# Optimization experiments

Hardware: AMD Instinct MI355X
Metric: run time of the kernel (lower is better)

The kernel has to match this reference:

```python
import jax, jax.numpy as jnp
import numpy as np

KSIZE = 15
SIGMA = 3.0
PAD = KSIZE // 2


def _gauss_kernel2d():
    g = jnp.arange(KSIZE, dtype=jnp.float32) - KSIZE // 2
    g = jnp.exp(-(g ** 2) / (2.0 * SIGMA * SIGMA))
    g = g / g.sum()
    return g[:, None] * g[None, :]  # [15,15]


def _depthwise_blur(x, k2):
    # x: [B,C,H,W]; 15x15 Gaussian applied per channel (matches per-channel F.conv2d loop)
    C = x.shape[1]
    kernel = jnp.broadcast_to(k2[None, None], (C, 1, KSIZE, KSIZE))
    return jax.lax.conv_general_dilated(
        x, kernel, window_strides=(1, 1), padding=[(PAD, PAD), (PAD, PAD)],
        feature_group_count=C, dimension_numbers=("NCHW", "OIHW", "NCHW"))


def setup_inputs() -> dict:
    key = jax.random.key(0)
    B, C, H, W = 4, 3, 1024, 1024
    x = jax.random.uniform(key, (B, C, H, W), dtype=jnp.float32)
    f32 = lambda v: jnp.asarray(v, dtype=jnp.float32)
    return {
        "x": x,
        "gains": jnp.array([1.1, 1.0, 0.9], dtype=jnp.float32),
        "gamma": f32(0.9),
        "shadow_boost": f32(0.1),
        "highlight_reduce": f32(0.1),
        "brightness": f32(0.05),
        "contrast": f32(1.1),
        "enhance_amount": f32(0.8),
        "softness": f32(0.6),
        "intensity": f32(0.3),
        "rotation": f32(30.0),
        "hardness": f32(2.0),
    }


def reference(x, gains, gamma, shadow_boost, highlight_reduce, brightness,
              contrast, enhance_amount, softness, intensity, rotation, hardness):
    B, C, H, W = x.shape
    k2 = _gauss_kernel2d()

    # WhiteBalanceAdjustment
    x = x * gains.reshape(1, C, 1, 1)
    # ToneCurveAdjustment
    x = jnp.power(x, gamma)
    # ShadowHighlightEnhancement
    hi = jax.nn.sigmoid((x - 0.5) * 10.0)
    x = jnp.clip(x + shadow_boost * (1.0 - hi) - highlight_reduce * hi, 0.0, 1.0)
    # GlobalBrightnessContrastAdjustment
    x = jnp.clip(contrast * (x - 0.5) + 0.5 + brightness, 0.0, 1.0)
    # LocalContrastEnhancement
    local_mean = _depthwise_blur(x, k2)
    x = x + enhance_amount * (x - local_mean)
    # SoftnessFilter
    blurred = _depthwise_blur(x, k2)
    x = softness * blurred + (1.0 - softness) * x
    # GradientNDAdjustment
    ys = jnp.linspace(-1.0, 1.0, H, dtype=jnp.float32)
    xs = jnp.linspace(-1.0, 1.0, W, dtype=jnp.float32)
    grid_y, grid_x = jnp.meshgrid(ys, xs, indexing="ij")
    theta = rotation * (np.pi / 180.0)
    grid_rot = grid_x * jnp.cos(theta) + grid_y * jnp.sin(theta)
    mask = jax.nn.sigmoid(-hardness * grid_rot)[None, None]  # [1,1,H,W]
    x = jnp.clip(x * (1.0 - intensity * mask), 0.0, 1.0)

    return jnp.clip(x, 0.0, 1.0)
```

## Files before the change

### kernel.cpp

```cpp
#include <hip/hip_runtime.h>
#include <math.h>

#define HH 1024
#define WW 1024
#define NPLANES 12
#define PLANE (HH * WW)
#define NTOT (NPLANES * PLANE)

#define TW 64
#define TH 64
#define HRA 78
#define RAWP 84
#define HBLP 68

#define TH2 128
#define HRB 142

struct W15 { float w[15]; };

__device__ inline float4 ld4z(const float* __restrict__ row, int x) {
    if (x >= 0 && x + 3 < WW) return *(const float4*)(row + x);
    float4 r; float* p = (float*)&r;
#pragma unroll
    for (int j = 0; j < 4; ++j) { int xx = x + j; p[j] = (xx >= 0 && xx < WW) ? row[xx] : 0.0f; }
    return r;
}

__device__ inline float chain1(float t, float gain, float gamma, float sb,
                               float hr, float br, float ct) {
    t = t * gain;
    t = __builtin_amdgcn_exp2f(gamma * __log2f(t));
    float hi = __fdividef(1.0f, 1.0f + __expf((0.5f - t) * 10.0f));
    t = t + sb * (1.0f - hi) - hr * hi;
    t = fminf(fmaxf(t, 0.0f), 1.0f);
    t = ct * (t - 0.5f) + 0.5f + br;
    return fminf(fmaxf(t, 0.0f), 1.0f);
}

__global__ __launch_bounds__(256) void k_chain_blur_lce(
    const float* __restrict__ x, float* __restrict__ dst,
    const float* __restrict__ gains,
    const float* __restrict__ pg, const float* __restrict__ psb,
    const float* __restrict__ phr, const float* __restrict__ pbr,
    const float* __restrict__ pct, const float* __restrict__ penh, W15 wk)
{
    __shared__ float raw[HRA * RAWP];
    __shared__ float hbl[HRA * HBLP];
    const int p   = blockIdx.z;
    const int x0  = blockIdx.x * TW;
    const int y0  = blockIdx.y * TH;
    const int tid = threadIdx.x;
    const float* plane = x + (size_t)p * PLANE;

    const float gain  = gains[p % 3];
    const float gamma = *pg, sb = *psb, hr = *phr, br = *pbr, ct = *pct;
    const float e     = *penh;

    for (int i = tid; i < HRA * 20; i += 256) {
        int r  = i / 20;
        int c4 = i % 20;
        int y  = y0 - 7 + r;
        int xb = x0 - 8 + c4 * 4;
        float4 v;
        if (y >= 0 && y < HH) {
            float4 f = ld4z(plane + (size_t)y * WW, xb);
            float* pf = (float*)&f; float* pv = (float*)&v;
#pragma unroll
            for (int j = 0; j < 4; ++j) {
                float cv = chain1(pf[j], gain, gamma, sb, hr, br, ct);
                int xx = xb + j;
                pv[j] = (xx >= 0 && xx < WW) ? cv : 0.0f;
            }
        } else {
            v = make_float4(0.0f, 0.0f, 0.0f, 0.0f);
        }
        *(float4*)&raw[r * RAWP + c4 * 4] = v;
    }
    __syncthreads();

    {
        const int c4 = (tid & 15) * 4;
        const int r0 = tid >> 4;
#pragma unroll
        for (int it = 0; it < 5; ++it) {
            int r = r0 + 16 * it;
            if (r < HRA) {
                float f[20];
#pragma unroll
                for (int m = 0; m < 5; ++m)
                    *(float4*)&f[4 * m] = *(const float4*)&raw[r * RAWP + c4 + 4 * m];
                float4 o; float* po = (float*)&o;
#pragma unroll
                for (int j = 0; j < 4; ++j) {
                    float acc = 0.0f;
#pragma unroll
                    for (int k = 0; k < 15; ++k) acc += wk.w[k] * f[j + 1 + k];
                    po[j] = acc;
                }
                *(float4*)&hbl[r * HBLP + c4] = o;
            }
        }
    }
    __syncthreads();

    const int tx  = tid & 63;
    const int ty  = tid >> 6;
    const int ly0 = ty * 16;

    float win[15];
#pragma unroll
    for (int k = 0; k < 15; ++k) win[k] = hbl[(ly0 + k) * HBLP + tx];

    float* dstP = dst + (size_t)p * PLANE;
#pragma unroll
    for (int j = 0; j < 16; ++j) {
        int y = y0 + ly0 + j;
        float lm = 0.0f;
#pragma unroll
        for (int k = 0; k < 15; ++k) lm += wk.w[k] * win[k];
        float c = raw[(ly0 + j + 7) * RAWP + tx + 8];
        dstP[(size_t)y * WW + x0 + tx] = (1.0f + e) * c - e * lm;
#pragma unroll
        for (int k = 0; k < 14; ++k) win[k] = win[k + 1];
        win[14] = hbl[(ly0 + j + 15) * HBLP + tx];
    }
}

__global__ __launch_bounds__(256) void k_blur_final(
    const float* __restrict__ src, float* __restrict__ dst,
    const float* __restrict__ psoft, const float* __restrict__ pint,
    const float* __restrict__ prot, const float* __restrict__ phard, W15 wk)
{
    __shared__ float hbl[HRB * HBLP];
    const int p   = blockIdx.z;
    const int x0  = blockIdx.x * TW;
    const int y0  = blockIdx.y * TH2;
    const int tid = threadIdx.x;
    const float* plane = src + (size_t)p * PLANE;

    {
        const int c4 = (tid & 15) * 4;
        const int r0 = tid >> 4;
#pragma unroll
        for (int it = 0; it < 9; ++it) {
            int r = r0 + 16 * it;
            if (r < HRB) {
                int y = y0 - 7 + r;
                float4 o;
                if (y >= 0 && y < HH) {
                    const float* row = plane + (size_t)y * WW;
                    int xb = x0 + c4 - 8;
                    float f[20];
                    *(float4*)&f[0]  = ld4z(row, xb);
                    *(float4*)&f[4]  = ld4z(row, xb + 4);
                    *(float4*)&f[8]  = ld4z(row, xb + 8);
                    *(float4*)&f[12] = ld4z(row, xb + 12);
                    *(float4*)&f[16] = ld4z(row, xb + 16);
                    float* po = (float*)&o;
#pragma unroll
                    for (int j = 0; j < 4; ++j) {
                        float acc = 0.0f;
#pragma unroll
                        for (int k = 0; k < 15; ++k) acc += wk.w[k] * f[j + 1 + k];
                        po[j] = acc;
                    }
                } else {
                    o = make_float4(0.0f, 0.0f, 0.0f, 0.0f);
                }
                *(float4*)&hbl[r * HBLP + c4] = o;
            }
        }
    }
    __syncthreads();

    const int tx  = tid & 63;
    const int ty  = tid >> 6;
    const int ly0 = ty * 32;
    const int x   = x0 + tx;

    const float s     = *psoft;
    const float inten = *pint;
    const float hard  = *phard;
    const float theta = (*prot) * 0.017453292519943295f;
    const float cth = __cosf(theta), sth = __sinf(theta);
    const float base = (-1.0f + 2.0f * (float)x * (1.0f / (float)(WW - 1))) * cth;

    float win[15];
#pragma unroll
    for (int k = 0; k < 15; ++k) win[k] = hbl[(ly0 + k) * HBLP + tx];

    float* dstP = dst + (size_t)p * PLANE;
#pragma unroll
    for (int j = 0; j < 32; ++j) {
        int y = y0 + ly0 + j;
        float bl = 0.0f;
#pragma unroll
        for (int k = 0; k < 15; ++k) bl += wk.w[k] * win[k];
        float c = plane[(size_t)y * WW + x];
        float v = s * bl + (1.0f - s) * c;
        float gy = -1.0f + 2.0f * (float)y * (1.0f / (float)(HH - 1));
        float mask = __fdividef(1.0f, 1.0f + __expf(hard * (base + gy * sth)));
        v = v * (1.0f - inten * mask);
        v = fminf(fmaxf(v, 0.0f), 1.0f);
        dstP[(size_t)y * WW + x] = v;
#pragma unroll
        for (int k = 0; k < 14; ++k) win[k] = win[k + 1];
        win[14] = hbl[(ly0 + j + 15) * HBLP + tx];
    }
}

extern "C" void kernel_launch(void* const* d_in, const int* in_sizes, int n_in,
                              void* d_out, int out_size, void* d_ws, size_t ws_size,
                              hipStream_t stream)
{
    const float* x       = (const float*)d_in[0];
    const float* gains   = (const float*)d_in[1];
    const float* p_gamma = (const float*)d_in[2];
    const float* p_sb    = (const float*)d_in[3];
    const float* p_hr    = (const float*)d_in[4];
    const float* p_br    = (const float*)d_in[5];
    const float* p_ct    = (const float*)d_in[6];
    const float* p_enh   = (const float*)d_in[7];
    const float* p_soft  = (const float*)d_in[8];
    const float* p_int   = (const float*)d_in[9];
    const float* p_rot   = (const float*)d_in[10];
    const float* p_hard  = (const float*)d_in[11];

    float* X2  = (float*)d_ws;
    float* OUT = (float*)d_out;

    W15 wk;
    {
        double g[15], sum = 0.0;
        for (int i = 0; i < 15; ++i) { double d = (double)(i - 7); g[i] = exp(-d * d / 18.0); sum += g[i]; }
        for (int i = 0; i < 15; ++i) wk.w[i] = (float)(g[i] / sum);
    }

    dim3 ga(WW / TW, HH / TH, NPLANES);
    k_chain_blur_lce<<<ga, dim3(256), 0, stream>>>(
        x, X2, gains, p_gamma, p_sb, p_hr, p_br, p_ct, p_enh, wk);

    dim3 gb(WW / TW, HH / TH2, NPLANES);
    k_blur_final<<<gb, dim3(256), 0, stream>>>(
        X2, OUT, p_soft, p_int, p_rot, p_hard, wk);
}
```

Baseline: 203.0 us.

## Fuse both blur stages into one kernel with halo recomputation in LDS

Merges the two kernels into a single kernel that computes the tone chain, the first blur and the local-contrast result for a tile with a 14-pixel halo, keeps that intermediate in shared memory, then applies the second blur and the final mask. This removes the global round trip of the intermediate image and one kernel launch. In exchange each 64x32 tile recomputes a large halo (60x96 raw region for 32 output rows), adding redundant chain and blur arithmetic, and uses more shared memory per block, which may limit occupancy.

```diff
diff --git a/kernel.cpp b/kernel.cpp
--- a/kernel.cpp
+++ b/kernel.cpp
@@ -5,16 +5,18 @@
 #define WW 1024
 #define NPLANES 12
 #define PLANE (HH * WW)
-#define NTOT (NPLANES * PLANE)
 
 #define TW 64
-#define TH 64
-#define HRA 78
-#define RAWP 84
-#define HBLP 68
-
-#define TH2 128
-#define HRB 142
+#define TH 32
+#define RAWR 60
+#define RAWC 24
+#define RAWP 100
+#define HB1R 60
+#define HB1P 80
+#define X2R  46
+#define X2P  80
+#define HB2R 46
+#define HB2P 68
 
 struct W15 { float w[15]; };
 
@@ -37,15 +39,20 @@
     return fminf(fmaxf(t, 0.0f), 1.0f);
 }
 
-__global__ __launch_bounds__(256) void k_chain_blur_lce(
-    const float* __restrict__ x, float* __restrict__ dst,
+__global__ __launch_bounds__(256, 2) void k_mega(
+    const float* __restrict__ x, float* __restrict__ out,
     const float* __restrict__ gains,
     const float* __restrict__ pg, const float* __restrict__ psb,
     const float* __restrict__ phr, const float* __restrict__ pbr,
-    const float* __restrict__ pct, const float* __restrict__ penh, W15 wk)
+    const float* __restrict__ pct, const float* __restrict__ penh,
+    const float* __restrict__ psoft, const float* __restrict__ pint,
+    const float* __restrict__ prot, const float* __restrict__ phard, W15 wk)
 {
-    __shared__ float raw[HRA * RAWP];
-    __shared__ float hbl[HRA * HBLP];
+    __shared__ float raw[RAWR * RAWP];
+    __shared__ float hb1[HB1R * HB1P];
+    __shared__ float x2 [X2R  * X2P ];
+    float* hb2 = raw;
+
     const int p   = blockIdx.z;
     const int x0  = blockIdx.x * TW;
     const int y0  = blockIdx.y * TH;
@@ -56,14 +63,14 @@
     const float gamma = *pg, sb = *psb, hr = *phr, br = *pbr, ct = *pct;
     const float e     = *penh;
 
-    for (int i = tid; i < HRA * 20; i += 256) {
-        int r  = i / 20;
-        int c4 = i % 20;
-        int y  = y0 - 7 + r;
-        int xb = x0 - 8 + c4 * 4;
+    for (int i = tid; i < RAWR * RAWC; i += 256) {
+        int r  = i / RAWC;
+        int cc = i - r * RAWC;
+        int gy = y0 - 14 + r;
+        int xb = x0 - 16 + cc * 4;
         float4 v;
-        if (y >= 0 && y < HH) {
-            float4 f = ld4z(plane + (size_t)y * WW, xb);
+        if (gy >= 0 && gy < HH) {
+            float4 f = ld4z(plane + (size_t)gy * WW, xb);
             float* pf = (float*)&f; float* pv = (float*)&v;
 #pragma unroll
             for (int j = 0; j < 4; ++j) {
@@ -74,7 +81,7 @@
         } else {
             v = make_float4(0.0f, 0.0f, 0.0f, 0.0f);
         }
-        *(float4*)&raw[r * RAWP + c4 * 4] = v;
+        *(float4*)&raw[r * RAWP + cc * 4] = v;
     }
     __syncthreads();
 
@@ -82,9 +89,9 @@
         const int c4 = (tid & 15) * 4;
         const int r0 = tid >> 4;
 #pragma unroll
-        for (int it = 0; it < 5; ++it) {
+        for (int it = 0; it < 4; ++it) {
             int r = r0 + 16 * it;
-            if (r < HRA) {
+            if (r < HB1R) {
                 float f[20];
 #pragma unroll
                 for (int m = 0; m < 5; ++m)
@@ -97,115 +104,119 @@
                     for (int k = 0; k < 15; ++k) acc += wk.w[k] * f[j + 1 + k];
                     po[j] = acc;
                 }
-                *(float4*)&hbl[r * HBLP + c4] = o;
-            }
-        }
-    }
-    __syncthreads();
-
-    const int tx  = tid & 63;
-    const int ty  = tid >> 6;
-    const int ly0 = ty * 16;
-
-    float win[15];
-#pragma unroll
-    for (int k = 0; k < 15; ++k) win[k] = hbl[(ly0 + k) * HBLP + tx];
-
-    float* dstP = dst + (size_t)p * PLANE;
-#pragma unroll
-    for (int j = 0; j < 16; ++j) {
-        int y = y0 + ly0 + j;
-        float lm = 0.0f;
-#pragma unroll
-        for (int k = 0; k < 15; ++k) lm += wk.w[k] * win[k];
-        float c = raw[(ly0 + j + 7) * RAWP + tx + 8];
-        dstP[(size_t)y * WW + x0 + tx] = (1.0f + e) * c - e * lm;
-#pragma unroll
-        for (int k = 0; k < 14; ++k) win[k] = win[k + 1];
-        win[14] = hbl[(ly0 + j + 15) * HBLP + tx];
-    }
-}
-
-__global__ __launch_bounds__(256) void k_blur_final(
-    const float* __restrict__ src, float* __restrict__ dst,
-    const float* __restrict__ psoft, const float* __restrict__ pint,
-    const float* __restrict__ prot, const float* __restrict__ phard, W15 wk)
-{
-    __shared__ float hbl[HRB * HBLP];
-    const int p   = blockIdx.z;
-    const int x0  = blockIdx.x * TW;
-    const int y0  = blockIdx.y * TH2;
-    const int tid = threadIdx.x;
-    const float* plane = src + (size_t)p * PLANE;
+                *(float4*)&hb1[r * HB1P + c4] = o;
+            }
+        }
+        const int cB = 64 + (tid & 3) * 4;
+        const int rB = tid >> 2;
+        if (rB < HB1R) {
+            float f[20];
+#pragma unroll
+            for (int m = 0; m < 5; ++m)
+                *(float4*)&f[4 * m] = *(const float4*)&raw[rB * RAWP + cB + 4 * m];
+            float4 o; float* po = (float*)&o;
+#pragma unroll
+            for (int j = 0; j < 4; ++j) {
+                float acc = 0.0f;
+#pragma unroll
+                for (int k = 0; k < 15; ++k) acc += wk.w[k] * f[j + 1 + k];
+                po[j] = acc;
+            }
+            *(float4*)&hb1[rB * HB1P + cB] = o;
+        }
+    }
+    __syncthreads();
+
+    if (tid < 240) {
+        const int band = tid / 80;
+        const int c    = tid - band * 80;
+        const int r0b  = band * 16;
+        const int gx   = x0 - 8 + c;
+        const bool colok = (gx >= 0) && (gx < WW);
+
+        float win[15];
+#pragma unroll
+        for (int k = 0; k < 14; ++k) win[k] = hb1[(r0b + k) * HB1P + c];
+
+#pragma unroll
+        for (int j = 0; j < 16; ++j) {
+            int rr = r0b + j;
+            if (rr < X2R) {
+                win[14] = hb1[(rr + 14) * HB1P + c];
+                float lm = 0.0f;
+#pragma unroll
+                for (int k = 0; k < 15; ++k) lm += wk.w[k] * win[k];
+                float t0c = raw[(rr + 7) * RAWP + c + 8];
+                float v = (1.0f + e) * t0c - e * lm;
+                int gy = y0 - 7 + rr;
+                x2[rr * X2P + c] = (colok && gy >= 0 && gy < HH) ? v : 0.0f;
+#pragma unroll
+                for (int k = 0; k < 14; ++k) win[k] = win[k + 1];
+            }
+        }
+    }
+    __syncthreads();
 
     {
         const int c4 = (tid & 15) * 4;
         const int r0 = tid >> 4;
 #pragma unroll
-        for (int it = 0; it < 9; ++it) {
+        for (int it = 0; it < 3; ++it) {
             int r = r0 + 16 * it;
-            if (r < HRB) {
-                int y = y0 - 7 + r;
-                float4 o;
-                if (y >= 0 && y < HH) {
-                    const float* row = plane + (size_t)y * WW;
-                    int xb = x0 + c4 - 8;
-                    float f[20];
-                    *(float4*)&f[0]  = ld4z(row, xb);
-                    *(float4*)&f[4]  = ld4z(row, xb + 4);
-                    *(float4*)&f[8]  = ld4z(row, xb + 8);
-                    *(float4*)&f[12] = ld4z(row, xb + 12);
-                    *(float4*)&f[16] = ld4z(row, xb + 16);
-                    float* po = (float*)&o;
-#pragma unroll
-                    for (int j = 0; j < 4; ++j) {
-                        float acc = 0.0f;
-#pragma unroll
-                        for (int k = 0; k < 15; ++k) acc += wk.w[k] * f[j + 1 + k];
-                        po[j] = acc;
-                    }
-                } else {
-                    o = make_float4(0.0f, 0.0f, 0.0f, 0.0f);
+            if (r < HB2R) {
+                float f[20];
+#pragma unroll
+                for (int m = 0; m < 5; ++m)
+                    *(float4*)&f[4 * m] = *(const float4*)&x2[r * X2P + c4 + 4 * m];
+                float4 o; float* po = (float*)&o;
+#pragma unroll
+                for (int j = 0; j < 4; ++j) {
+                    float acc = 0.0f;
+#pragma unroll
+                    for (int k = 0; k < 15; ++k) acc += wk.w[k] * f[j + 1 + k];
+                    po[j] = acc;
                 }
-                *(float4*)&hbl[r * HBLP + c4] = o;
-            }
-        }
-    }
-    __syncthreads();
-
-    const int tx  = tid & 63;
-    const int ty  = tid >> 6;
-    const int ly0 = ty * 32;
-    const int x   = x0 + tx;
-
-    const float s     = *psoft;
-    const float inten = *pint;
-    const float hard  = *phard;
-    const float theta = (*prot) * 0.017453292519943295f;
-    const float cth = __cosf(theta), sth = __sinf(theta);
-    const float base = (-1.0f + 2.0f * (float)x * (1.0f / (float)(WW - 1))) * cth;
-
-    float win[15];
-#pragma unroll
-    for (int k = 0; k < 15; ++k) win[k] = hbl[(ly0 + k) * HBLP + tx];
-
-    float* dstP = dst + (size_t)p * PLANE;
-#pragma unroll
-    for (int j = 0; j < 32; ++j) {
-        int y = y0 + ly0 + j;
-        float bl = 0.0f;
-#pragma unroll
-        for (int k = 0; k < 15; ++k) bl += wk.w[k] * win[k];
-        float c = plane[(size_t)y * WW + x];
-        float v = s * bl + (1.0f - s) * c;
-        float gy = -1.0f + 2.0f * (float)y * (1.0f / (float)(HH - 1));
-        float mask = __fdividef(1.0f, 1.0f + __expf(hard * (base + gy * sth)));
-        v = v * (1.0f - inten * mask);
-        v = fminf(fmaxf(v, 0.0f), 1.0f);
-        dstP[(size_t)y * WW + x] = v;
-#pragma unroll
-        for (int k = 0; k < 14; ++k) win[k] = win[k + 1];
-        win[14] = hbl[(ly0 + j + 15) * HBLP + tx];
+                *(float4*)&hb2[r * HB2P + c4] = o;
+            }
+        }
+    }
+    __syncthreads();
+
+    {
+        const int tx  = tid & 63;
+        const int ty  = tid >> 6;
+        const int ly0 = ty * 8;
+        const int gx  = x0 + tx;
+
+        const float s     = *psoft;
+        const float inten = *pint;
+        const float hard  = *phard;
+        const float theta = (*prot) * 0.017453292519943295f;
+        const float cth = __cosf(theta), sth = __sinf(theta);
+        const float base = (-1.0f + 2.0f * (float)gx * (1.0f / (float)(WW - 1))) * cth;
+
+        float win[15];
+#pragma unroll
+        for (int k = 0; k < 14; ++k) win[k] = hb2[(ly0 + k) * HB2P + tx];
+
+        float* dstP = out + (size_t)p * PLANE;
+#pragma unroll
+        for (int j = 0; j < 8; ++j) {
+            win[14] = hb2[(ly0 + j + 14) * HB2P + tx];
+            float bl = 0.0f;
+#pragma unroll
+            for (int k = 0; k < 15; ++k) bl += wk.w[k] * win[k];
+            float c = x2[(ly0 + j + 7) * X2P + tx + 8];
+            float v = s * bl + (1.0f - s) * c;
+            int gy = y0 + ly0 + j;
+            float gyf = -1.0f + 2.0f * (float)gy * (1.0f / (float)(HH - 1));
+            float mask = __fdividef(1.0f, 1.0f + __expf(hard * (base + gyf * sth)));
+            v = v * (1.0f - inten * mask);
+            v = fminf(fmaxf(v, 0.0f), 1.0f);
+            dstP[(size_t)gy * WW + gx] = v;
+#pragma unroll
+            for (int k = 0; k < 14; ++k) win[k] = win[k + 1];
+        }
     }
 }
 
@@ -226,9 +237,6 @@
     const float* p_rot   = (const float*)d_in[10];
     const float* p_hard  = (const float*)d_in[11];
 
-    float* X2  = (float*)d_ws;
-    float* OUT = (float*)d_out;
-
     W15 wk;
     {
         double g[15], sum = 0.0;
@@ -236,11 +244,8 @@
         for (int i = 0; i < 15; ++i) wk.w[i] = (float)(g[i] / sum);
     }
 
-    dim3 ga(WW / TW, HH / TH, NPLANES);
-    k_chain_blur_lce<<<ga, dim3(256), 0, stream>>>(
-        x, X2, gains, p_gamma, p_sb, p_hr, p_br, p_ct, p_enh, wk);
-
-    dim3 gb(WW / TW, HH / TH2, NPLANES);
-    k_blur_final<<<gb, dim3(256), 0, stream>>>(
-        X2, OUT, p_soft, p_int, p_rot, p_hard, wk);
-}
+    dim3 grid(WW / TW, HH / TH, NPLANES);
+    k_mega<<<grid, dim3(256), 0, stream>>>(
+        x, (float*)d_out, gains, p_gamma, p_sb, p_hr, p_br, p_ct,
+        p_enh, p_soft, p_int, p_rot, p_hard, wk);
+}
```

Measured after the change: 260.9 us. 1.29x slower.

## Fuse chain into horizontal blur registers and add interior fast paths

Applied to the files above, without the earlier changes.

The first kernel no longer stages chain-processed pixels in a shared raw tile. Each thread loads its 20-wide halo row from global memory, applies the tone chain in registers, and computes the horizontal blur directly, storing centre values separately. Both kernels gain a bounds-check-free path for interior tiles, and the second kernel's tile height is reduced to 64 rows. This removes one shared-memory pass and a barrier, but recomputes the transcendental chain about four times per pixel and increases vertical halo overhead in the second kernel.

```diff
diff --git a/kernel.cpp b/kernel.cpp
--- a/kernel.cpp
+++ b/kernel.cpp
@@ -5,16 +5,11 @@
 #define WW 1024
 #define NPLANES 12
 #define PLANE (HH * WW)
-#define NTOT (NPLANES * PLANE)
 
 #define TW 64
 #define TH 64
-#define HRA 78
-#define RAWP 84
-#define HBLP 68
-
-#define TH2 128
-#define HRB 142
+#define HR 78
+#define PITCH 68
 
 struct W15 { float w[15]; };
 
@@ -37,15 +32,27 @@
     return fminf(fmaxf(t, 0.0f), 1.0f);
 }
 
-__global__ __launch_bounds__(256) void k_chain_blur_lce(
-    const float* __restrict__ x, float* __restrict__ dst,
+__device__ inline float4 hdot4(const float f[20], const W15& wk) {
+    float4 o; float* po = (float*)&o;
+#pragma unroll
+    for (int j = 0; j < 4; ++j) {
+        float acc = 0.0f;
+#pragma unroll
+        for (int k = 0; k < 15; ++k) acc += wk.w[k] * f[j + 1 + k];
+        po[j] = acc;
+    }
+    return o;
+}
+
+__global__ __launch_bounds__(256) void k_chain_lce(
+    const float* __restrict__ x, float* __restrict__ x2o,
     const float* __restrict__ gains,
     const float* __restrict__ pg, const float* __restrict__ psb,
     const float* __restrict__ phr, const float* __restrict__ pbr,
     const float* __restrict__ pct, const float* __restrict__ penh, W15 wk)
 {
-    __shared__ float raw[HRA * RAWP];
-    __shared__ float hbl[HRA * HBLP];
+    __shared__ float hbl[HR * PITCH];
+    __shared__ float t0s[TH * PITCH];
     const int p   = blockIdx.z;
     const int x0  = blockIdx.x * TW;
     const int y0  = blockIdx.y * TH;
@@ -56,118 +63,56 @@
     const float gamma = *pg, sb = *psb, hr = *phr, br = *pbr, ct = *pct;
     const float e     = *penh;
 
-    for (int i = tid; i < HRA * 20; i += 256) {
-        int r  = i / 20;
-        int c4 = i % 20;
-        int y  = y0 - 7 + r;
-        int xb = x0 - 8 + c4 * 4;
-        float4 v;
-        if (y >= 0 && y < HH) {
-            float4 f = ld4z(plane + (size_t)y * WW, xb);
-            float* pf = (float*)&f; float* pv = (float*)&v;
-#pragma unroll
-            for (int j = 0; j < 4; ++j) {
-                float cv = chain1(pf[j], gain, gamma, sb, hr, br, ct);
-                int xx = xb + j;
-                pv[j] = (xx >= 0 && xx < WW) ? cv : 0.0f;
-            }
-        } else {
-            v = make_float4(0.0f, 0.0f, 0.0f, 0.0f);
-        }
-        *(float4*)&raw[r * RAWP + c4 * 4] = v;
-    }
-    __syncthreads();
-
-    {
-        const int c4 = (tid & 15) * 4;
-        const int r0 = tid >> 4;
-#pragma unroll
-        for (int it = 0; it < 5; ++it) {
-            int r = r0 + 16 * it;
-            if (r < HRA) {
+    const bool edge = (blockIdx.x == 0) || (blockIdx.x == WW / TW - 1) ||
+                      (blockIdx.y == 0) || (blockIdx.y == HH / TH - 1);
+    const int cx = (tid & 15) * 4;
+    const int r0 = tid >> 4;
+
+    if (!edge) {
+#pragma unroll
+        for (int it = 0; it < 5; ++it) {
+            int r = r0 + 16 * it;
+            if (r < HR) {
+                const float* rp = plane + (size_t)(y0 - 7 + r) * WW + (x0 + cx - 8);
                 float f[20];
-#pragma unroll
-                for (int m = 0; m < 5; ++m)
-                    *(float4*)&f[4 * m] = *(const float4*)&raw[r * RAWP + c4 + 4 * m];
-                float4 o; float* po = (float*)&o;
-#pragma unroll
-                for (int j = 0; j < 4; ++j) {
-                    float acc = 0.0f;
-#pragma unroll
-                    for (int k = 0; k < 15; ++k) acc += wk.w[k] * f[j + 1 + k];
-                    po[j] = acc;
-                }
-                *(float4*)&hbl[r * HBLP + c4] = o;
-            }
-        }
-    }
-    __syncthreads();
-
-    const int tx  = tid & 63;
-    const int ty  = tid >> 6;
-    const int ly0 = ty * 16;
-
-    float win[15];
-#pragma unroll
-    for (int k = 0; k < 15; ++k) win[k] = hbl[(ly0 + k) * HBLP + tx];
-
-    float* dstP = dst + (size_t)p * PLANE;
-#pragma unroll
-    for (int j = 0; j < 16; ++j) {
-        int y = y0 + ly0 + j;
-        float lm = 0.0f;
-#pragma unroll
-        for (int k = 0; k < 15; ++k) lm += wk.w[k] * win[k];
-        float c = raw[(ly0 + j + 7) * RAWP + tx + 8];
-        dstP[(size_t)y * WW + x0 + tx] = (1.0f + e) * c - e * lm;
-#pragma unroll
-        for (int k = 0; k < 14; ++k) win[k] = win[k + 1];
-        win[14] = hbl[(ly0 + j + 15) * HBLP + tx];
-    }
-}
-
-__global__ __launch_bounds__(256) void k_blur_final(
-    const float* __restrict__ src, float* __restrict__ dst,
-    const float* __restrict__ psoft, const float* __restrict__ pint,
-    const float* __restrict__ prot, const float* __restrict__ phard, W15 wk)
-{
-    __shared__ float hbl[HRB * HBLP];
-    const int p   = blockIdx.z;
-    const int x0  = blockIdx.x * TW;
-    const int y0  = blockIdx.y * TH2;
-    const int tid = threadIdx.x;
-    const float* plane = src + (size_t)p * PLANE;
-
-    {
-        const int c4 = (tid & 15) * 4;
-        const int r0 = tid >> 4;
-#pragma unroll
-        for (int it = 0; it < 9; ++it) {
-            int r = r0 + 16 * it;
-            if (r < HRB) {
-                int y = y0 - 7 + r;
+                *(float4*)&f[0]  = *(const float4*)(rp);
+                *(float4*)&f[4]  = *(const float4*)(rp + 4);
+                *(float4*)&f[8]  = *(const float4*)(rp + 8);
+                *(float4*)&f[12] = *(const float4*)(rp + 12);
+                *(float4*)&f[16] = *(const float4*)(rp + 16);
+#pragma unroll
+                for (int m = 0; m < 20; ++m) f[m] = chain1(f[m], gain, gamma, sb, hr, br, ct);
+                if (r >= 7 && r < 7 + TH) *(float4*)&t0s[(r - 7) * PITCH + cx] = *(float4*)&f[8];
+                *(float4*)&hbl[r * PITCH + cx] = hdot4(f, wk);
+            }
+        }
+    } else {
+        for (int it = 0; it < 5; ++it) {
+            int r = r0 + 16 * it;
+            if (r < HR) {
+                int gy = y0 - 7 + r;
                 float4 o;
-                if (y >= 0 && y < HH) {
-                    const float* row = plane + (size_t)y * WW;
-                    int xb = x0 + c4 - 8;
+                if (gy >= 0 && gy < HH) {
+                    const float* row = plane + (size_t)gy * WW;
+                    int xb = x0 + cx - 8;
                     float f[20];
                     *(float4*)&f[0]  = ld4z(row, xb);
                     *(float4*)&f[4]  = ld4z(row, xb + 4);
                     *(float4*)&f[8]  = ld4z(row, xb + 8);
                     *(float4*)&f[12] = ld4z(row, xb + 12);
                     *(float4*)&f[16] = ld4z(row, xb + 16);
-                    float* po = (float*)&o;
-#pragma unroll
-                    for (int j = 0; j < 4; ++j) {
-                        float acc = 0.0f;
-#pragma unroll
-                        for (int k = 0; k < 15; ++k) acc += wk.w[k] * f[j + 1 + k];
-                        po[j] = acc;
+#pragma unroll
+                    for (int m = 0; m < 20; ++m) {
+                        float cv = chain1(f[m], gain, gamma, sb, hr, br, ct);
+                        int xx = xb + m;
+                        f[m] = (xx >= 0 && xx < WW) ? cv : 0.0f;
                     }
+                    if (r >= 7 && r < 7 + TH) *(float4*)&t0s[(r - 7) * PITCH + cx] = *(float4*)&f[8];
+                    o = hdot4(f, wk);
                 } else {
                     o = make_float4(0.0f, 0.0f, 0.0f, 0.0f);
                 }
-                *(float4*)&hbl[r * HBLP + c4] = o;
+                *(float4*)&hbl[r * PITCH + cx] = o;
             }
         }
     }
@@ -175,37 +120,117 @@
 
     const int tx  = tid & 63;
     const int ty  = tid >> 6;
-    const int ly0 = ty * 32;
-    const int x   = x0 + tx;
+    const int ly0 = ty * 16;
+
+    float win[15];
+#pragma unroll
+    for (int k = 0; k < 15; ++k) win[k] = hbl[(ly0 + k) * PITCH + tx];
+
+    float* dstP = x2o + (size_t)p * PLANE;
+#pragma unroll
+    for (int j = 0; j < 16; ++j) {
+        int y = y0 + ly0 + j;
+        float lm = 0.0f;
+#pragma unroll
+        for (int k = 0; k < 15; ++k) lm += wk.w[k] * win[k];
+        float c = t0s[(ly0 + j) * PITCH + tx];
+        dstP[(size_t)y * WW + x0 + tx] = (1.0f + e) * c - e * lm;
+#pragma unroll
+        for (int k = 0; k < 14; ++k) win[k] = win[k + 1];
+        win[14] = hbl[(ly0 + j + 15) * PITCH + tx];
+    }
+}
+
+__global__ __launch_bounds__(256) void k_blur_final(
+    const float* __restrict__ src, float* __restrict__ dst,
+    const float* __restrict__ psoft, const float* __restrict__ pint,
+    const float* __restrict__ prot, const float* __restrict__ phard, W15 wk)
+{
+    __shared__ float hbl[HR * PITCH];
+    const int p   = blockIdx.z;
+    const int x0  = blockIdx.x * TW;
+    const int y0  = blockIdx.y * TH;
+    const int tid = threadIdx.x;
+    const float* plane = src + (size_t)p * PLANE;
+
+    const bool edge = (blockIdx.x == 0) || (blockIdx.x == WW / TW - 1) ||
+                      (blockIdx.y == 0) || (blockIdx.y == HH / TH - 1);
+    const int cx = (tid & 15) * 4;
+    const int r0 = tid >> 4;
+
+    if (!edge) {
+#pragma unroll
+        for (int it = 0; it < 5; ++it) {
+            int r = r0 + 16 * it;
+            if (r < HR) {
+                const float* rp = plane + (size_t)(y0 - 7 + r) * WW + (x0 + cx - 8);
+                float f[20];
+                *(float4*)&f[0]  = *(const float4*)(rp);
+                *(float4*)&f[4]  = *(const float4*)(rp + 4);
+                *(float4*)&f[8]  = *(const float4*)(rp + 8);
+                *(float4*)&f[12] = *(const float4*)(rp + 12);
+                *(float4*)&f[16] = *(const float4*)(rp + 16);
+                *(float4*)&hbl[r * PITCH + cx] = hdot4(f, wk);
+            }
+        }
+    } else {
+        for (int it = 0; it < 5; ++it) {
+            int r = r0 + 16 * it;
+            if (r < HR) {
+                int gy = y0 - 7 + r;
+                float4 o;
+                if (gy >= 0 && gy < HH) {
+                    const float* row = plane + (size_t)gy * WW;
+                    int xb = x0 + cx - 8;
+                    float f[20];
+                    *(float4*)&f[0]  = ld4z(row, xb);
+                    *(float4*)&f[4]  = ld4z(row, xb + 4);
+                    *(float4*)&f[8]  = ld4z(row, xb + 8);
+                    *(float4*)&f[12] = ld4z(row, xb + 12);
+                    *(float4*)&f[16] = ld4z(row, xb + 16);
+                    o = hdot4(f, wk);
+                } else {
+                    o = make_float4(0.0f, 0.0f, 0.0f, 0.0f);
+                }
+                *(float4*)&hbl[r * PITCH + cx] = o;
+            }
+        }
+    }
+    __syncthreads();
+
+    const int tx  = tid & 63;
+    const int ty  = tid >> 6;
+    const int ly0 = ty * 16;
+    const int gx  = x0 + tx;
 
     const float s     = *psoft;
     const float inten = *pint;
     const float hard  = *phard;
     const float theta = (*prot) * 0.017453292519943295f;
     const float cth = __cosf(theta), sth = __sinf(theta);
-    const float base = (-1.0f + 2.0f * (float)x * (1.0f / (float)(WW - 1))) * cth;
+    const float base = (-1.0f + 2.0f * (float)gx * (1.0f / (float)(WW - 1))) * cth;
 
     float win[15];
 #pragma unroll
-    for (int k = 0; k < 15; ++k) win[k] = hbl[(ly0 + k) * HBLP + tx];
+    for (int k = 0; k < 15; ++k) win[k] = hbl[(ly0 + k) * PITCH + tx];
 
     float* dstP = dst + (size_t)p * PLANE;
 #pragma unroll
-    for (int j = 0; j < 32; ++j) {
+    for (int j = 0; j < 16; ++j) {
         int y = y0 + ly0 + j;
         float bl = 0.0f;
 #pragma unroll
         for (int k = 0; k < 15; ++k) bl += wk.w[k] * win[k];
-        float c = plane[(size_t)y * WW + x];
+        float c = plane[(size_t)y * WW + gx];
         float v = s * bl + (1.0f - s) * c;
-        float gy = -1.0f + 2.0f * (float)y * (1.0f / (float)(HH - 1));
-        float mask = __fdividef(1.0f, 1.0f + __expf(hard * (base + gy * sth)));
+        float gyf = -1.0f + 2.0f * (float)y * (1.0f / (float)(HH - 1));
+        float mask = __fdividef(1.0f, 1.0f + __expf(hard * (base + gyf * sth)));
         v = v * (1.0f - inten * mask);
         v = fminf(fmaxf(v, 0.0f), 1.0f);
-        dstP[(size_t)y * WW + x] = v;
+        dstP[(size_t)y * WW + gx] = v;
 #pragma unroll
         for (int k = 0; k < 14; ++k) win[k] = win[k + 1];
-        win[14] = hbl[(ly0 + j + 15) * HBLP + tx];
+        win[14] = hbl[(ly0 + j + 15) * PITCH + tx];
     }
 }
 
@@ -236,11 +261,9 @@
         for (int i = 0; i < 15; ++i) wk.w[i] = (float)(g[i] / sum);
     }
 
-    dim3 ga(WW / TW, HH / TH, NPLANES);
-    k_chain_blur_lce<<<ga, dim3(256), 0, stream>>>(
+    dim3 grid(WW / TW, HH / TH, NPLANES);
+    k_chain_lce<<<grid, dim3(256), 0, stream>>>(
         x, X2, gains, p_gamma, p_sb, p_hr, p_br, p_ct, p_enh, wk);
-
-    dim3 gb(WW / TW, HH / TH2, NPLANES);
-    k_blur_final<<<gb, dim3(256), 0, stream>>>(
+    k_blur_final<<<grid, dim3(256), 0, stream>>>(
         X2, OUT, p_soft, p_int, p_rot, p_hard, wk);
 }
```

New measurement: 219.6 us. 1.08x slower.
